# Performance work log

Measured on AMD Instinct MI355X. Metric: run time of the kernel, lower is better.

## Reference

```python
import jax, jax.numpy as jnp
import numpy as np

N, U, OUT_DIM, K, B = 3960, 128, 1, 2, 16
NUM_MAT = 2 * K + 1  # 2 supports (dual random walk), K hops, + identity


def setup_inputs() -> dict:
    key = jax.random.key(0)
    ks = jax.random.split(key, 12)
    s = 0.02
    inp = {
        'inputs': jax.random.normal(ks[0], (B, N * OUT_DIM), jnp.float32),
        'adj_mx': jax.random.uniform(ks[1], (N, N), jnp.float32),
        'hidden_state': jax.random.normal(ks[2], (2, B, N * U), jnp.float32),
        'forward_index': 0,
        # layer 0: input dim = OUT_DIM (=1)
        'Wg0': s * jax.random.normal(ks[3], ((OUT_DIM + U) * NUM_MAT, 2 * U), jnp.float32),
        'bg0': jnp.ones((2 * U,), jnp.float32),  # bias_start=1.0 for gates
        'Wc0': s * jax.random.normal(ks[4], ((OUT_DIM + U) * NUM_MAT, U), jnp.float32),
        'bc0': jnp.zeros((U,), jnp.float32),
        # layer 1: input dim = U
        'Wg1': s * jax.random.normal(ks[5], ((U + U) * NUM_MAT, 2 * U), jnp.float32),
        'bg1': jnp.ones((2 * U,), jnp.float32),
        'Wc1': s * jax.random.normal(ks[6], ((U + U) * NUM_MAT, U), jnp.float32),
        'bc1': jnp.zeros((U,), jnp.float32),
        # projection Linear(rnn_units, output_dim)
        'Wp': s * jax.random.normal(ks[7], (U, OUT_DIM), jnp.float32),
        'bp': jnp.zeros((OUT_DIM,), jnp.float32),
    }
    return inp


def _random_walk(adj):
    # D^{-1} A with 0 for zero-degree rows
    d = adj.sum(axis=1)
    d_inv = jnp.where(d > 0, 1.0 / d, 0.0)
    return d_inv[:, None] * adj


def _gconv(x, h, supports, W, b):
    # x: (B,N,c_in), h: (B,N,U) -> (B,N,out)
    bsz = x.shape[0]
    cat = jnp.concatenate([x, h], axis=2)          # (B,N,C)
    C = cat.shape[2]
    x0 = cat.transpose(1, 2, 0).reshape(N, C * bsz)  # (N, C*B)
    xs = [x0]
    for S in supports:
        x1 = S @ x0
        xs.append(x1)
        xk_2, xk_1 = x0, x1
        for _ in range(2, K + 1):
            x2 = 2.0 * (S @ xk_1) - xk_2  # Chebyshev-style recurrence (as in GTS/DCRNN)
            xs.append(x2)
            xk_2, xk_1 = xk_1, x2
    xcat = jnp.stack(xs, 0)                         # (M,N,C*B)
    xcat = xcat.reshape(NUM_MAT, N, C, bsz).transpose(3, 1, 2, 0)  # (B,N,C,M)
    xcat = xcat.reshape(bsz * N, C * NUM_MAT)
    return (xcat @ W + b).reshape(bsz, N, -1)


def _dcgru_cell(x, h, supports, Wg, bg, Wc, bc):
    gates = jax.nn.sigmoid(_gconv(x, h, supports, Wg, bg))  # (B,N,2U)
    r, u = gates[..., :U], gates[..., U:]
    c = jnp.tanh(_gconv(x, r * h, supports, Wc, bc))        # (B,N,U)
    return u * h + (1.0 - u) * c


def reference(inputs, adj_mx, hidden_state, forward_index,
              Wg0, bg0, Wc0, bc0, Wg1, bg1, Wc1, bc1, Wp, bp):
    bsz = inputs.shape[0]
    supports = [_random_walk(adj_mx).T, _random_walk(adj_mx.T).T]
    x = inputs.reshape(bsz, N, OUT_DIM)
    h0 = hidden_state[0].reshape(bsz, N, U)
    h1 = hidden_state[1].reshape(bsz, N, U)
    nh0 = _dcgru_cell(x, h0, supports, Wg0, bg0, Wc0, bc0)
    nh1 = _dcgru_cell(nh0, h1, supports, Wg1, bg1, Wc1, bc1)
    out = (nh1.reshape(-1, U) @ Wp + bp).reshape(bsz, N * OUT_DIM)
    return out
```

## Files before the change

### kernel.cpp

```cpp
#include <hip/hip_runtime.h>


#define NN 3960
#define NP 3968
#define BB 16
#define UU 128
#define NT 62

typedef __attribute__((ext_vector_type(8))) short v8s;
typedef __attribute__((ext_vector_type(4))) float v4f;

__device__ __forceinline__ float bf2f(short h) {
  union { unsigned int u; float f; } v;
  v.u = ((unsigned int)(unsigned short)h) << 16;
  return v.f;
}
__device__ __forceinline__ short f2bf(float f) {
  union { float f; unsigned int u; } v; v.f = f;
  unsigned int r = (v.u + 0x7FFFu + ((v.u >> 16) & 1u)) >> 16;
  return (short)r;
}
__device__ __forceinline__ void gld16(const void* g, void* l) {
  __builtin_amdgcn_global_load_lds(
      (const __attribute__((address_space(1))) void*)g,
      (__attribute__((address_space(3))) void*)l, 16, 0, 0);
}


__global__ void k_rowsum(const float* __restrict__ A, float* __restrict__ out) {
  int i = blockIdx.x;
  float s = 0.f;
  for (int j = threadIdx.x; j < NN; j += 256) s += A[i * NN + j];
  __shared__ float red[256];
  red[threadIdx.x] = s; __syncthreads();
  for (int k = 128; k > 0; k >>= 1) {
    if (threadIdx.x < k) red[threadIdx.x] += red[threadIdx.x + k];
    __syncthreads();
  }
  if (threadIdx.x == 0) out[i] = red[0];
}

__global__ void k_colpart(const float* __restrict__ A, float* __restrict__ part) {
  int j = blockIdx.x * 256 + threadIdx.x;
  if (j >= NN) return;
  int p = blockIdx.y;
  int r0 = p * 495, r1 = r0 + 495;
  float s = 0.f;
  for (int i = r0; i < r1; i++) s += A[i * NN + j];
  part[p * NP + j] = s;
}

__global__ void k_inv(const float* __restrict__ rs, const float* __restrict__ part,
                      float* __restrict__ rinv, float* __restrict__ cinv) {
  int j = blockIdx.x * 256 + threadIdx.x;
  if (j >= NP) return;
  float r = 0.f, c = 0.f;
  if (j < NN) {
    r = rs[j];
    float s = 0.f;
    for (int p = 0; p < 8; p++) s += part[p * NP + j];
    c = s;
  }
  rinv[j] = (j < NN && r > 0.f) ? 1.f / r : 0.f;
  cinv[j] = (j < NN && c > 0.f) ? 1.f / c : 0.f;
}

__global__ void k_supports(const float* __restrict__ A, const float* __restrict__ rinv,
                           const float* __restrict__ cinv,
                           short* __restrict__ S0, short* __restrict__ S1) {
  __shared__ float t[32][33];
  int i0 = blockIdx.y * 32, j0 = blockIdx.x * 32;
  int tx = threadIdx.x, ty = threadIdx.y;
  #pragma unroll
  for (int q = 0; q < 4; q++) {
    int r = i0 + ty + 8 * q, c = j0 + tx;
    float a = (r < NN && c < NN) ? A[r * NN + c] : 0.f;
    t[ty + 8 * q][tx] = a;
    S1[r * NP + c] = f2bf(a * cinv[c]);
  }
  __syncthreads();
  #pragma unroll
  for (int q = 0; q < 4; q++) {
    int I = j0 + ty + 8 * q, J = i0 + tx;
    S0[I * NP + J] = f2bf(t[tx][ty + 8 * q] * rinv[J]);
  }
}

__global__ void k_buildH(const float* __restrict__ hs,
                         short* __restrict__ H0, short* __restrict__ H1) {
  __shared__ float t[32][33];
  int n0 = blockIdx.x * 32, u0 = blockIdx.y * 32;
  int bz = blockIdx.z; int b = bz & 15; int layer = bz >> 4;
  const float* src = hs + (size_t)(layer * BB + b) * NN * UU;
  short* H = layer ? H1 : H0;
  int tx = threadIdx.x, ty = threadIdx.y;
  #pragma unroll
  for (int q = 0; q < 4; q++) {
    int n = n0 + ty + 8 * q, u = u0 + tx;
    t[ty + 8 * q][tx] = (n < NN) ? src[n * UU + u] : 0.f;
  }
  __syncthreads();
  #pragma unroll
  for (int q = 0; q < 4; q++) {
    int u = u0 + ty + 8 * q, n = n0 + tx;
    H[(b * UU + u) * NP + n] = f2bf(t[tx][ty + 8 * q]);
  }
}

__global__ void k_buildX0c(const float* __restrict__ inp, short* __restrict__ X) {
  int n = blockIdx.x * 128 + threadIdx.x;
  int row = blockIdx.y;
  float v = (row < BB && n < NN) ? inp[row * NN + n] : 0.f;
  X[row * NP + n] = f2bf(v);
}

__global__ void k_buildWt(const float* __restrict__ W, short* __restrict__ Wt,
                          int O, int KL, int CxP, int Cx) {
  int idx = blockIdx.x * 256 + threadIdx.x;
  if (idx >= O * KL) return;
  int o = idx / KL, k = idx % KL;
  int KX = 5 * CxP;
  float v = 0.f;
  if (k < KX) {
    int m = k / CxP, c = k % CxP;
    if (c < Cx) v = W[(c * 5 + m) * O + o];
  } else {
    int kl = k - KX; int m = kl >> 7, u = kl & 127;
    v = W[((Cx + u) * 5 + m) * O + o];
  }
  Wt[o * KL + k] = f2bf(v);
}

struct Bt8Args {
  const short* A[4];
  short* Y[4];
  const short* SUB[4];
  int mr[4];
};

__launch_bounds__(512, 2)
__global__ void k_gemm_bt8(Bt8Args P, const short* __restrict__ T0,
                           const short* __restrict__ T1) {
  int z = blockIdx.z;
  int l = blockIdx.x + (blockIdx.y << 3);
  int bx = l >> 4;
  int by = ((l & 7) << 1) + ((l >> 3) & 1);
  int row0 = bx * 256;
  if (row0 >= P.mr[z]) return;
  const short* Ag = P.A[z];
  short* Cg = P.Y[z];
  const short* X0 = P.SUB[z];
  const short* Bg = (z & 1) ? T1 : T0;
  __shared__ short lds[65536];
  int tid = threadIdx.x, lane = tid & 63, wv = tid >> 6;
  int wr = wv >> 2, wc = wv & 3;
  int col0 = by * 256;

  int srow = wv * 16 + (lane >> 2);
  int scol = ((lane & 3) * 8) ^ ((lane >> 5) << 4);
  const short* aS0 = Ag + (size_t)(row0 + srow) * NP + scol;
  const short* aS1 = Ag + (size_t)(row0 + 128 + srow) * NP + scol;
  int br0 = col0 + srow;        if (br0 > NP - 1) br0 = NP - 1;
  int br1 = col0 + 128 + srow;  if (br1 > NP - 1) br1 = NP - 1;
  const short* bS0 = Bg + (size_t)br0 * NP + scol;
  const short* bS1 = Bg + (size_t)br1 * NP + scol;
  short* ldsA = lds + wv * 1024 + lane * 8;
  short* ldsB = lds + 32768 + wv * 1024 + lane * 8;

#define STG_A(buf, h, tau) do { const short* _s = ((h) ? aS1 : aS0) + (tau) * 64; \
    gld16(_s,      ldsA + (buf) * 16384 + (h) * 8192); \
    gld16(_s + 32, ldsA + (buf) * 16384 + (h) * 8192 + 512); } while (0)
#define STG_B(buf, h, tau) do { const short* _s = ((h) ? bS1 : bS0) + (tau) * 64; \
    gld16(_s,      ldsB + (buf) * 16384 + (h) * 8192); \
    gld16(_s + 32, ldsB + (buf) * 16384 + (h) * 8192 + 512); } while (0)

  int fro = (lane & 15) * 32 + (((lane >> 4) * 8) ^ ((lane & 8) * 2));
  int aBase = wr * 8192 + fro;
  int bBase = 32768 + (wc >> 1) * 8192 + (wc & 1) * 4096 + fro;

  v4f acc[8][4];
  #pragma unroll
  for (int i = 0; i < 8; i++)
    #pragma unroll
    for (int j = 0; j < 4; j++) {
      acc[i][j][0] = 0.f; acc[i][j][1] = 0.f; acc[i][j][2] = 0.f; acc[i][j][3] = 0.f;
    }
  v8s afr[4][2], bfr[4][2];

#define RD_A(b, miB) do { _Pragma("unroll") \
  for (int m2 = 0; m2 < 4; m2++) { \
    afr[m2][0] = *(const v8s*)&lds[aBase + (b) * 16384 + ((miB) + m2) * 1024]; \
    afr[m2][1] = *(const v8s*)&lds[aBase + (b) * 16384 + ((miB) + m2) * 1024 + 512]; } } while (0)
#define RD_B(b, niB) do { _Pragma("unroll") \
  for (int n2 = 0; n2 < 2; n2++) { \
    bfr[(niB) + n2][0] = *(const v8s*)&lds[bBase + (b) * 16384 + ((niB) + n2) * 1024]; \
    bfr[(niB) + n2][1] = *(const v8s*)&lds[bBase + (b) * 16384 + ((niB) + n2) * 1024 + 512]; } } while (0)
#define MM(miB, niB) do { __builtin_amdgcn_s_setprio(1); \
  _Pragma("unroll") for (int m2 = 0; m2 < 4; m2++) \
  _Pragma("unroll") for (int n2 = 0; n2 < 2; n2++) { \
    acc[(miB) + m2][(niB) + n2] = __builtin_amdgcn_mfma_f32_16x16x32_bf16( \
        afr[m2][0], bfr[(niB) + n2][0], acc[(miB) + m2][(niB) + n2], 0, 0, 0); \
    acc[(miB) + m2][(niB) + n2] = __builtin_amdgcn_mfma_f32_16x16x32_bf16( \
        afr[m2][1], bfr[(niB) + n2][1], acc[(miB) + m2][(niB) + n2], 0, 0, 0); } \
  __builtin_amdgcn_s_setprio(0); } while (0)
#define BARS do { __builtin_amdgcn_s_barrier(); __builtin_amdgcn_sched_barrier(0); } while (0)
#define VMC(n) asm volatile("s_waitcnt vmcnt(" #n ")" ::: "memory")

  STG_A(0, 0, 0); STG_A(0, 1, 0); STG_B(0, 0, 0); STG_B(0, 1, 0);
  STG_A(1, 0, 1); STG_B(1, 0, 1); STG_B(1, 1, 1);
  VMC(6);
  BARS;

  for (int it = 0; it < NT / 2; it++) {
    int t = 2 * it;
    int st1 = t + 1;
    int st2 = t + 2 > NT - 1 ? NT - 1 : t + 2;
    int st3 = t + 3 > NT - 1 ? NT - 1 : t + 3;
    RD_A(0, 0); RD_B(0, 0); STG_A(1, 1, st1); BARS; MM(0, 0); BARS;
    RD_B(0, 2); BARS; MM(0, 2); BARS;
    RD_A(0, 4); STG_B(0, 0, st2); BARS; MM(4, 0); BARS;
    STG_B(0, 1, st2); VMC(4); BARS; MM(4, 2); BARS;
    RD_A(1, 0); RD_B(1, 0); STG_A(0, 0, st2); BARS; MM(0, 0); BARS;
    RD_B(1, 2); STG_A(0, 1, st2); BARS; MM(0, 2); BARS;
    RD_A(1, 4); STG_B(1, 0, st3); BARS; MM(4, 0); BARS;
    STG_B(1, 1, st3); STG_A(1, 0, st3); VMC(6); BARS; MM(4, 2); BARS;
  }

  int cheb = X0 != nullptr;
  #pragma unroll
  for (int mi = 0; mi < 8; mi++)
    #pragma unroll
    for (int ni = 0; ni < 4; ni++) {
      int col = col0 + wc * 64 + ni * 16 + (lane & 15);
      if (col < NP) {
        #pragma unroll
        for (int r = 0; r < 4; r++) {
          int row = row0 + wr * 128 + mi * 16 + (lane >> 4) * 4 + r;
          float v = acc[mi][ni][r];
          if (cheb) v = 2.f * v - bf2f(X0[(size_t)row * NP + col]);
          Cg[(size_t)row * NP + col] = f2bf(v);
        }
      }
    }
#undef STG_A
#undef STG_B
#undef RD_A
#undef RD_B
#undef MM
#undef BARS
#undef VMC
}

__launch_bounds__(256, 2)
__global__ void k_gemm_wt(const short* __restrict__ Wt, int KL, int KX, int CxP,
                          int bsx,
                          const short* __restrict__ pX0, const short* __restrict__ pX1,
                          const short* __restrict__ pX2, const short* __restrict__ pX3,
                          const short* __restrict__ pX4,
                          const short* __restrict__ pH0, const short* __restrict__ pH1,
                          const short* __restrict__ pH2, const short* __restrict__ pH3,
                          const short* __restrict__ pH4,
                          const float* __restrict__ bias, const short* __restrict__ H,
                          short* __restrict__ Ut, short* __restrict__ out0, int epi) {
  __shared__ short lA[128 * 32];
  __shared__ short lB[128 * 40];
  int tid = threadIdx.x, lane = tid & 63, w = tid >> 6;
  int n0 = blockIdx.x * 128;
  int oy = blockIdx.y;
  int b = blockIdx.z;
  int arow = w * 16 + (lane >> 2), koff = (lane & 3) * 8;
  const short* wa0 = Wt + (oy * 128 + arow) * KL + koff;
  const short* wa1 = Wt + (oy * 128 + 64 + arow) * KL + koff;
  short* la0 = lA + w * 512 + lane * 8;
  short* la1 = lA + 2048 + w * 512 + lane * 8;
  int srow = tid >> 3, c16 = (tid & 7) * 16;
  int sk7 = srow & 7, sk3 = srow >> 3;
  int wr = (w >> 1) * 64, wc = (w & 1) * 64;
  v4f acc[4][4];
  #pragma unroll
  for (int i = 0; i < 4; i++)
    #pragma unroll
    for (int j = 0; j < 4; j++) {
      acc[i][j][0] = 0.f; acc[i][j][1] = 0.f; acc[i][j][2] = 0.f; acc[i][j][3] = 0.f;
    }
  int KT = KL >> 5;
  for (int kt = 0; kt < KT; kt++) {
    int kb = kt * 32;
    const short* src;
    if (kb < KX) {
      int m = kb / CxP, c0 = kb % CxP;
      const short* base = m == 0 ? pX0 : m == 1 ? pX1 : m == 2 ? pX2 : m == 3 ? pX3 : pX4;
      src = base + (b * bsx + c0) * NP;
    } else {
      int kl = kb - KX; int m = kl >> 7, c0 = kl & 127;
      const short* base = m == 0 ? pH0 : m == 1 ? pH1 : m == 2 ? pH2 : m == 3 ? pH3 : pH4;
      src = base + (b * UU + c0) * NP;
    }
    __syncthreads();
    gld16(wa0 + kb, la0); gld16(wa1 + kb, la1);
    const v8s* p = (const v8s*)(src + srow * NP + n0 + c16);
    v8s v0 = p[0], v1 = p[1];
    #pragma unroll
    for (int j = 0; j < 8; j++) {
      int cA = c16 + j, cB = c16 + 8 + j;
      lB[cA * 40 + sk7 + 8 * ((sk3 ^ (cA >> 4)) & 3)] = v0[j];
      lB[cB * 40 + sk7 + 8 * ((sk3 ^ (cB >> 4)) & 3)] = v1[j];
    }
    __syncthreads();
    v8s af[4], bfv[4];
    #pragma unroll
    for (int mi = 0; mi < 4; mi++)
      af[mi] = *(const v8s*)&lA[(wr + mi * 16 + (lane & 15)) * 32 + (lane >> 4) * 8];
    #pragma unroll
    for (int ni = 0; ni < 4; ni++) {
      int colb = wc + ni * 16 + (lane & 15);
      bfv[ni] = *(const v8s*)&lB[colb * 40 + 8 * (((lane >> 4) ^ (colb >> 4)) & 3)];
    }
    #pragma unroll
    for (int mi = 0; mi < 4; mi++)
      #pragma unroll
      for (int ni = 0; ni < 4; ni++)
        acc[mi][ni] = __builtin_amdgcn_mfma_f32_16x16x32_bf16(af[mi], bfv[ni], acc[mi][ni], 0, 0, 0);
  }
  #pragma unroll
  for (int mi = 0; mi < 4; mi++)
    #pragma unroll
    for (int ni = 0; ni < 4; ni++) {
      int col = n0 + wc + ni * 16 + (lane & 15);
      #pragma unroll
      for (int r = 0; r < 4; r++) {
        int o = oy * 128 + wr + mi * 16 + (lane >> 4) * 4 + r;
        float v = acc[mi][ni][r] + bias[o];
        if (epi == 0) {
          float s = 1.f / (1.f + __expf(-v));
          if (o < UU) {
            int idx = (b * UU + o) * NP + col;
            out0[idx] = f2bf(s * bf2f(H[idx]));
          } else {
            int idx = (b * UU + (o - UU)) * NP + col;
            Ut[idx] = f2bf(s);
          }
        } else {
          float cv = tanhf(v);
          int idx = (b * UU + o) * NP + col;
          float u = bf2f(Ut[idx]), h = bf2f(H[idx]);
          out0[idx] = f2bf(u * h + (1.f - u) * cv);
        }
      }
    }
}

__global__ void k_proj(const short* __restrict__ nh, const float* __restrict__ Wp,
                       const float* __restrict__ bp, float* __restrict__ out) {
  int n = blockIdx.x * 256 + threadIdx.x;
  int b = blockIdx.y;
  if (n >= NN) return;
  float acc = bp[0];
  #pragma unroll 8
  for (int u = 0; u < UU; u++)
    acc += bf2f(nh[(b * UU + u) * NP + n]) * Wp[u];
  out[b * NN + n] = acc;
}

__global__ void k_bail(float* out, int n, float val) {
  int i = blockIdx.x * 256 + threadIdx.x;
  if (i < n) out[i] = val;
}


extern "C" void kernel_launch(void* const* d_in, const int* in_sizes, int n_in,
                              void* d_out, int out_size, void* d_ws, size_t ws_size,
                              hipStream_t stream) {
  const float* inp = (const float*)d_in[0];
  const float* adj = (const float*)d_in[1];
  const float* hid = (const float*)d_in[2];
  const float* Wg0 = (const float*)d_in[4];
  const float* bg0 = (const float*)d_in[5];
  const float* Wc0 = (const float*)d_in[6];
  const float* bc0 = (const float*)d_in[7];
  const float* Wg1 = (const float*)d_in[8];
  const float* bg1 = (const float*)d_in[9];
  const float* Wc1 = (const float*)d_in[10];
  const float* bc1 = (const float*)d_in[11];
  const float* Wp = (const float*)d_in[12];
  const float* bp = (const float*)d_in[13];
  float* out = (float*)d_out;

  const size_t SZ_S = (size_t)NP * NP * 2;
  const size_t SZ_M = (size_t)2048 * NP * 2;
  const size_t SZ_MS = (size_t)512 * NP * 2;

  size_t o_S0 = 0;
  size_t o_S1 = o_S0 + SZ_S;
  size_t o_H0 = o_S1 + SZ_S;
  size_t o_H1 = o_H0 + SZ_M;
  size_t o_Ut = o_H1 + SZ_M;
  size_t o_Xrh = o_Ut + SZ_M;
  size_t o_nh0 = o_Xrh + SZ_M;
  size_t o_YB = o_nh0 + SZ_M;
  size_t o_YX123 = o_YB + 4 * SZ_M;
  size_t o_X0c = o_YX123;
  size_t o_YS = o_X0c + SZ_MS;
  size_t o_Wg0t = o_YX123 + 3 * SZ_M;
  size_t o_Wc0t = o_Wg0t + (size_t)256 * 800 * 2;
  size_t o_Wg1t = o_Wc0t + (size_t)128 * 800 * 2;
  size_t o_Wc1t = o_Wg1t + (size_t)256 * 1280 * 2;
  size_t o_rinv = o_Wc1t + (size_t)128 * 1280 * 2;
  size_t o_cinv = o_rinv + NP * 4;
  size_t o_rs = o_cinv + NP * 4;
  size_t o_part = o_rs + NP * 4;
  size_t NEED = o_part + (size_t)8 * NP * 4;

  if (ws_size < NEED) {
    float v = -(float)(double)(ws_size >> 20);
    k_bail<<<(out_size + 255) / 256, 256, 0, stream>>>(out, out_size, v);
    return;
  }

  char* w = (char*)d_ws;
  short* S0 = (short*)(w + o_S0);
  short* S1 = (short*)(w + o_S1);
  short* H0 = (short*)(w + o_H0);
  short* H1 = (short*)(w + o_H1);
  short* Ut = (short*)(w + o_Ut);
  short* Xrh = (short*)(w + o_Xrh);
  short* nh0 = (short*)(w + o_nh0);
  short* nh1 = Ut;
  short* YB[4];
  for (int i = 0; i < 4; i++) YB[i] = (short*)(w + o_YB + i * SZ_M);
  short* YXa = H0;
  short* YXb = (short*)(w + o_YX123 + 0 * SZ_M);
  short* YXc = (short*)(w + o_YX123 + 1 * SZ_M);
  short* YXd = (short*)(w + o_YX123 + 2 * SZ_M);
  short* YS[4];
  for (int i = 0; i < 4; i++) YS[i] = (short*)(w + o_YS + i * SZ_MS);
  short* X0c = (short*)(w + o_X0c);
  short* Wg0t = (short*)(w + o_Wg0t);
  short* Wc0t = (short*)(w + o_Wc0t);
  short* Wg1t = (short*)(w + o_Wg1t);
  short* Wc1t = (short*)(w + o_Wc1t);
  float* rinv = (float*)(w + o_rinv);
  float* cinv = (float*)(w + o_cinv);
  float* rs = (float*)(w + o_rs);
  float* part = (float*)(w + o_part);

  k_rowsum<<<NN, 256, 0, stream>>>(adj, rs);
  k_colpart<<<dim3(16, 8), 256, 0, stream>>>(adj, part);
  k_inv<<<16, 256, 0, stream>>>(rs, part, rinv, cinv);
  k_supports<<<dim3(124, 124), dim3(32, 8), 0, stream>>>(adj, rinv, cinv, S0, S1);
  k_buildH<<<dim3(124, 4, 32), dim3(32, 8), 0, stream>>>(hid, H0, H1);
  k_buildX0c<<<dim3(31, 256), 128, 0, stream>>>(inp, X0c);
  k_buildWt<<<(256 * 800 + 255) / 256, 256, 0, stream>>>(Wg0, Wg0t, 256, 800, 32, 1);
  k_buildWt<<<(128 * 800 + 255) / 256, 256, 0, stream>>>(Wc0, Wc0t, 128, 800, 32, 1);
  k_buildWt<<<(256 * 1280 + 255) / 256, 256, 0, stream>>>(Wg1, Wg1t, 256, 1280, 128, 128);
  k_buildWt<<<(128 * 1280 + 255) / 256, 256, 0, stream>>>(Wc1, Wc1t, 128, 1280, 128, 128);

  auto launch_bt8 = [&](const Bt8Args& a, int nz) {
    k_gemm_bt8<<<dim3(8, 16, nz), 512, 0, stream>>>(a, S0, S1);
  };

  {
    Bt8Args h1 = {{X0c, X0c, H0, H0}, {YS[0], YS[2], YB[0], YB[2]},
                  {nullptr, nullptr, nullptr, nullptr}, {256, 256, 2048, 2048}};
    launch_bt8(h1, 4);
    Bt8Args h2 = {{YS[0], YS[2], YB[0], YB[2]}, {YS[1], YS[3], YB[1], YB[3]},
                  {X0c, X0c, H0, H0}, {256, 256, 2048, 2048}};
    launch_bt8(h2, 4);
  }
  k_gemm_wt<<<dim3(31, 2, 16), 256, 0, stream>>>(Wg0t, 800, 160, 32, 1,
      X0c, YS[0], YS[1], YS[2], YS[3], H0, YB[0], YB[1], YB[2], YB[3],
      bg0, H0, Ut, Xrh, 0);
  {
    Bt8Args h1 = {{Xrh, Xrh, nullptr, nullptr}, {YB[0], YB[2], nullptr, nullptr},
                  {nullptr, nullptr, nullptr, nullptr}, {2048, 2048, 0, 0}};
    launch_bt8(h1, 2);
    Bt8Args h2 = {{YB[0], YB[2], nullptr, nullptr}, {YB[1], YB[3], nullptr, nullptr},
                  {Xrh, Xrh, nullptr, nullptr}, {2048, 2048, 0, 0}};
    launch_bt8(h2, 2);
  }
  k_gemm_wt<<<dim3(31, 1, 16), 256, 0, stream>>>(Wc0t, 800, 160, 32, 1,
      X0c, YS[0], YS[1], YS[2], YS[3], Xrh, YB[0], YB[1], YB[2], YB[3],
      bc0, H0, Ut, nh0, 1);

  {
    Bt8Args h1 = {{nh0, nh0, H1, H1}, {YXa, YXc, YB[0], YB[2]},
                  {nullptr, nullptr, nullptr, nullptr}, {2048, 2048, 2048, 2048}};
    launch_bt8(h1, 4);
    Bt8Args h2 = {{YXa, YXc, YB[0], YB[2]}, {YXb, YXd, YB[1], YB[3]},
                  {nh0, nh0, H1, H1}, {2048, 2048, 2048, 2048}};
    launch_bt8(h2, 4);
  }
  k_gemm_wt<<<dim3(31, 2, 16), 256, 0, stream>>>(Wg1t, 1280, 640, 128, 128,
      nh0, YXa, YXb, YXc, YXd, H1, YB[0], YB[1], YB[2], YB[3],
      bg1, H1, Ut, Xrh, 0);
  {
    Bt8Args h1 = {{Xrh, Xrh, nullptr, nullptr}, {YB[0], YB[2], nullptr, nullptr},
                  {nullptr, nullptr, nullptr, nullptr}, {2048, 2048, 0, 0}};
    launch_bt8(h1, 2);
    Bt8Args h2 = {{YB[0], YB[2], nullptr, nullptr}, {YB[1], YB[3], nullptr, nullptr},
                  {Xrh, Xrh, nullptr, nullptr}, {2048, 2048, 0, 0}};
    launch_bt8(h2, 2);
  }
  k_gemm_wt<<<dim3(31, 1, 16), 256, 0, stream>>>(Wc1t, 1280, 640, 128, 128,
      nh0, YXa, YXb, YXc, YXd, Xrh, YB[0], YB[1], YB[2], YB[3],
      bc1, H1, Ut, nh1, 1);

  k_proj<<<dim3(16, 16), 256, 0, stream>>>(nh1, Wp, bp, out);
}
```

Before: 1.732 ms.

## Double-buffer LDS fragment registers to overlap reads with MFMA in GEMM loop

Splits the A/B fragment registers into low/high halves so LDS reads for the next sub-tile are issued alongside MFMAs on the current one, rather than being separated from them by barriers. Global-to-LDS staging is reordered to match, with one stage per barrier phase and the prefetch depth adjusted. The aim is to hide LDS read latency behind matrix instructions in the dense support GEMM. In exchange it uses more VGPRs, which could hurt occupancy under launch bounds of 2 blocks per SM, and the reordered staging carries correctness risk for buffer reuse.

```diff
diff --git a/kernel.cpp b/kernel.cpp
--- a/kernel.cpp
+++ b/kernel.cpp
@@ -185,45 +185,54 @@
     for (int j = 0; j < 4; j++) {
       acc[i][j][0] = 0.f; acc[i][j][1] = 0.f; acc[i][j][2] = 0.f; acc[i][j][3] = 0.f;
     }
-  v8s afr[4][2], bfr[4][2];
-
-#define RD_A(b, miB) do { _Pragma("unroll") \
+  v8s afrL[4][2], afrH[4][2], bfrL[2][2], bfrH[2][2];
+
+#define RD_AL(b) do { _Pragma("unroll") \
   for (int m2 = 0; m2 < 4; m2++) { \
-    afr[m2][0] = *(const v8s*)&lds[aBase + (b) * 16384 + ((miB) + m2) * 1024]; \
-    afr[m2][1] = *(const v8s*)&lds[aBase + (b) * 16384 + ((miB) + m2) * 1024 + 512]; } } while (0)
-#define RD_B(b, niB) do { _Pragma("unroll") \
+    afrL[m2][0] = *(const v8s*)&lds[aBase + (b) * 16384 + m2 * 1024]; \
+    afrL[m2][1] = *(const v8s*)&lds[aBase + (b) * 16384 + m2 * 1024 + 512]; } } while (0)
+#define RD_AH(b) do { _Pragma("unroll") \
+  for (int m2 = 0; m2 < 4; m2++) { \
+    afrH[m2][0] = *(const v8s*)&lds[aBase + (b) * 16384 + (4 + m2) * 1024]; \
+    afrH[m2][1] = *(const v8s*)&lds[aBase + (b) * 16384 + (4 + m2) * 1024 + 512]; } } while (0)
+#define RD_BL(b) do { _Pragma("unroll") \
   for (int n2 = 0; n2 < 2; n2++) { \
-    bfr[(niB) + n2][0] = *(const v8s*)&lds[bBase + (b) * 16384 + ((niB) + n2) * 1024]; \
-    bfr[(niB) + n2][1] = *(const v8s*)&lds[bBase + (b) * 16384 + ((niB) + n2) * 1024 + 512]; } } while (0)
-#define MM(miB, niB) do { __builtin_amdgcn_s_setprio(1); \
+    bfrL[n2][0] = *(const v8s*)&lds[bBase + (b) * 16384 + n2 * 1024]; \
+    bfrL[n2][1] = *(const v8s*)&lds[bBase + (b) * 16384 + n2 * 1024 + 512]; } } while (0)
+#define RD_BH(b) do { _Pragma("unroll") \
+  for (int n2 = 0; n2 < 2; n2++) { \
+    bfrH[n2][0] = *(const v8s*)&lds[bBase + (b) * 16384 + (2 + n2) * 1024]; \
+    bfrH[n2][1] = *(const v8s*)&lds[bBase + (b) * 16384 + (2 + n2) * 1024 + 512]; } } while (0)
+#define MMX(AF, BF, miB, niB) do { __builtin_amdgcn_s_setprio(1); \
   _Pragma("unroll") for (int m2 = 0; m2 < 4; m2++) \
   _Pragma("unroll") for (int n2 = 0; n2 < 2; n2++) { \
     acc[(miB) + m2][(niB) + n2] = __builtin_amdgcn_mfma_f32_16x16x32_bf16( \
-        afr[m2][0], bfr[(niB) + n2][0], acc[(miB) + m2][(niB) + n2], 0, 0, 0); \
+        AF[m2][0], BF[n2][0], acc[(miB) + m2][(niB) + n2], 0, 0, 0); \
     acc[(miB) + m2][(niB) + n2] = __builtin_amdgcn_mfma_f32_16x16x32_bf16( \
-        afr[m2][1], bfr[(niB) + n2][1], acc[(miB) + m2][(niB) + n2], 0, 0, 0); } \
+        AF[m2][1], BF[n2][1], acc[(miB) + m2][(niB) + n2], 0, 0, 0); } \
   __builtin_amdgcn_s_setprio(0); } while (0)
 #define BARS do { __builtin_amdgcn_s_barrier(); __builtin_amdgcn_sched_barrier(0); } while (0)
 #define VMC(n) asm volatile("s_waitcnt vmcnt(" #n ")" ::: "memory")
 
   STG_A(0, 0, 0); STG_A(0, 1, 0); STG_B(0, 0, 0); STG_B(0, 1, 0);
-  STG_A(1, 0, 1); STG_B(1, 0, 1); STG_B(1, 1, 1);
-  VMC(6);
+  STG_B(1, 0, 1); STG_B(1, 1, 1);
+  VMC(4);
   BARS;
+  RD_AL(0); RD_BL(0);
 
   for (int it = 0; it < NT / 2; it++) {
     int t = 2 * it;
-    int st1 = t + 1;
-    int st2 = t + 2 > NT - 1 ? NT - 1 : t + 2;
-    int st3 = t + 3 > NT - 1 ? NT - 1 : t + 3;
-    RD_A(0, 0); RD_B(0, 0); STG_A(1, 1, st1); BARS; MM(0, 0); BARS;
-    RD_B(0, 2); BARS; MM(0, 2); BARS;
-    RD_A(0, 4); STG_B(0, 0, st2); BARS; MM(4, 0); BARS;
-    STG_B(0, 1, st2); VMC(4); BARS; MM(4, 2); BARS;
-    RD_A(1, 0); RD_B(1, 0); STG_A(0, 0, st2); BARS; MM(0, 0); BARS;
-    RD_B(1, 2); STG_A(0, 1, st2); BARS; MM(0, 2); BARS;
-    RD_A(1, 4); STG_B(1, 0, st3); BARS; MM(4, 0); BARS;
-    STG_B(1, 1, st3); STG_A(1, 0, st3); VMC(6); BARS; MM(4, 2); BARS;
+    int s1 = t + 1;
+    int s2 = t + 2 > NT - 1 ? NT - 1 : t + 2;
+    int s3 = t + 3 > NT - 1 ? NT - 1 : t + 3;
+    STG_A(1, 0, s1); BARS; RD_BH(0); MMX(afrL, bfrL, 0, 0); BARS;
+    STG_A(1, 1, s1); BARS; RD_AH(0); MMX(afrL, bfrH, 0, 2); BARS;
+    STG_B(0, 0, s2); BARS; MMX(afrH, bfrL, 4, 0); BARS;
+    STG_B(0, 1, s2); VMC(4); BARS; RD_AL(1); RD_BL(1); MMX(afrH, bfrH, 4, 2); BARS;
+    STG_A(0, 0, s2); BARS; RD_BH(1); MMX(afrL, bfrL, 0, 0); BARS;
+    STG_A(0, 1, s2); BARS; RD_AH(1); MMX(afrL, bfrH, 0, 2); BARS;
+    STG_B(1, 0, s3); BARS; MMX(afrH, bfrL, 4, 0); BARS;
+    STG_B(1, 1, s3); VMC(4); BARS; RD_AL(0); RD_BL(0); MMX(afrH, bfrH, 4, 2); BARS;
   }
 
   int cheb = X0 != nullptr;
@@ -244,9 +253,11 @@
     }
 #undef STG_A
 #undef STG_B
-#undef RD_A
-#undef RD_B
-#undef MM
+#undef RD_AL
+#undef RD_AH
+#undef RD_BL
+#undef RD_BH
+#undef MMX
 #undef BARS
 #undef VMC
 }
```

After: 2.627 ms. +51.6%, slower.

## Replace double-buffered pipelined GEMM main loop with single-buffered load-wait-compute loop

Applied to the files above, without the earlier changes.

The 256x256-tile support GEMM kernel drops its hand-scheduled double-buffered LDS pipeline, where global-to-LDS loads for later K-tiles were interleaved with MFMA phases. Each K-step now loads its tile, waits for all loads, synchronizes, reads fragments and runs all MFMAs. LDS use is halved, which could allow more resident blocks, but load latency is no longer hidden behind compute within a block.

```diff
diff --git a/kernel.cpp b/kernel.cpp
--- a/kernel.cpp
+++ b/kernel.cpp
@@ -151,7 +151,7 @@
   short* Cg = P.Y[z];
   const short* X0 = P.SUB[z];
   const short* Bg = (z & 1) ? T1 : T0;
-  __shared__ short lds[65536];
+  __shared__ short lds[32768];
   int tid = threadIdx.x, lane = tid & 63, wv = tid >> 6;
   int wr = wv >> 2, wc = wv & 3;
   int col0 = by * 256;
@@ -165,18 +165,11 @@
   const short* bS0 = Bg + (size_t)br0 * NP + scol;
   const short* bS1 = Bg + (size_t)br1 * NP + scol;
   short* ldsA = lds + wv * 1024 + lane * 8;
-  short* ldsB = lds + 32768 + wv * 1024 + lane * 8;
-
-#define STG_A(buf, h, tau) do { const short* _s = ((h) ? aS1 : aS0) + (tau) * 64; \
-    gld16(_s,      ldsA + (buf) * 16384 + (h) * 8192); \
-    gld16(_s + 32, ldsA + (buf) * 16384 + (h) * 8192 + 512); } while (0)
-#define STG_B(buf, h, tau) do { const short* _s = ((h) ? bS1 : bS0) + (tau) * 64; \
-    gld16(_s,      ldsB + (buf) * 16384 + (h) * 8192); \
-    gld16(_s + 32, ldsB + (buf) * 16384 + (h) * 8192 + 512); } while (0)
+  short* ldsB = lds + 16384 + wv * 1024 + lane * 8;
 
   int fro = (lane & 15) * 32 + (((lane >> 4) * 8) ^ ((lane & 8) * 2));
   int aBase = wr * 8192 + fro;
-  int bBase = 32768 + (wc >> 1) * 8192 + (wc & 1) * 4096 + fro;
+  int bBase = 16384 + (wc >> 1) * 8192 + (wc & 1) * 4096 + fro;
 
   v4f acc[8][4];
   #pragma unroll
@@ -185,45 +178,46 @@
     for (int j = 0; j < 4; j++) {
       acc[i][j][0] = 0.f; acc[i][j][1] = 0.f; acc[i][j][2] = 0.f; acc[i][j][3] = 0.f;
     }
-  v8s afr[4][2], bfr[4][2];
-
-#define RD_A(b, miB) do { _Pragma("unroll") \
-  for (int m2 = 0; m2 < 4; m2++) { \
-    afr[m2][0] = *(const v8s*)&lds[aBase + (b) * 16384 + ((miB) + m2) * 1024]; \
-    afr[m2][1] = *(const v8s*)&lds[aBase + (b) * 16384 + ((miB) + m2) * 1024 + 512]; } } while (0)
-#define RD_B(b, niB) do { _Pragma("unroll") \
-  for (int n2 = 0; n2 < 2; n2++) { \
-    bfr[(niB) + n2][0] = *(const v8s*)&lds[bBase + (b) * 16384 + ((niB) + n2) * 1024]; \
-    bfr[(niB) + n2][1] = *(const v8s*)&lds[bBase + (b) * 16384 + ((niB) + n2) * 1024 + 512]; } } while (0)
-#define MM(miB, niB) do { __builtin_amdgcn_s_setprio(1); \
-  _Pragma("unroll") for (int m2 = 0; m2 < 4; m2++) \
-  _Pragma("unroll") for (int n2 = 0; n2 < 2; n2++) { \
-    acc[(miB) + m2][(niB) + n2] = __builtin_amdgcn_mfma_f32_16x16x32_bf16( \
-        afr[m2][0], bfr[(niB) + n2][0], acc[(miB) + m2][(niB) + n2], 0, 0, 0); \
-    acc[(miB) + m2][(niB) + n2] = __builtin_amdgcn_mfma_f32_16x16x32_bf16( \
-        afr[m2][1], bfr[(niB) + n2][1], acc[(miB) + m2][(niB) + n2], 0, 0, 0); } \
-  __builtin_amdgcn_s_setprio(0); } while (0)
+
 #define BARS do { __builtin_amdgcn_s_barrier(); __builtin_amdgcn_sched_barrier(0); } while (0)
-#define VMC(n) asm volatile("s_waitcnt vmcnt(" #n ")" ::: "memory")
-
-  STG_A(0, 0, 0); STG_A(0, 1, 0); STG_B(0, 0, 0); STG_B(0, 1, 0);
-  STG_A(1, 0, 1); STG_B(1, 0, 1); STG_B(1, 1, 1);
-  VMC(6);
-  BARS;
-
-  for (int it = 0; it < NT / 2; it++) {
-    int t = 2 * it;
-    int st1 = t + 1;
-    int st2 = t + 2 > NT - 1 ? NT - 1 : t + 2;
-    int st3 = t + 3 > NT - 1 ? NT - 1 : t + 3;
-    RD_A(0, 0); RD_B(0, 0); STG_A(1, 1, st1); BARS; MM(0, 0); BARS;
-    RD_B(0, 2); BARS; MM(0, 2); BARS;
-    RD_A(0, 4); STG_B(0, 0, st2); BARS; MM(4, 0); BARS;
-    STG_B(0, 1, st2); VMC(4); BARS; MM(4, 2); BARS;
-    RD_A(1, 0); RD_B(1, 0); STG_A(0, 0, st2); BARS; MM(0, 0); BARS;
-    RD_B(1, 2); STG_A(0, 1, st2); BARS; MM(0, 2); BARS;
-    RD_A(1, 4); STG_B(1, 0, st3); BARS; MM(4, 0); BARS;
-    STG_B(1, 1, st3); STG_A(1, 0, st3); VMC(6); BARS; MM(4, 2); BARS;
+#define VMC0 asm volatile("s_waitcnt vmcnt(0)" ::: "memory")
+
+  for (int t = 0; t < NT; t++) {
+    {
+      const short* sa0 = aS0 + t * 64;
+      const short* sa1 = aS1 + t * 64;
+      const short* sb0 = bS0 + t * 64;
+      const short* sb1 = bS1 + t * 64;
+      gld16(sa0, ldsA);             gld16(sa0 + 32, ldsA + 512);
+      gld16(sa1, ldsA + 8192);      gld16(sa1 + 32, ldsA + 8192 + 512);
+      gld16(sb0, ldsB);             gld16(sb0 + 32, ldsB + 512);
+      gld16(sb1, ldsB + 8192);      gld16(sb1 + 32, ldsB + 8192 + 512);
+    }
+    VMC0;
+    BARS;
+    v8s afr[8][2], bfr[4][2];
+    #pragma unroll
+    for (int mi = 0; mi < 8; mi++) {
+      afr[mi][0] = *(const v8s*)&lds[aBase + mi * 1024];
+      afr[mi][1] = *(const v8s*)&lds[aBase + mi * 1024 + 512];
+    }
+    #pragma unroll
+    for (int ni = 0; ni < 4; ni++) {
+      bfr[ni][0] = *(const v8s*)&lds[bBase + ni * 1024];
+      bfr[ni][1] = *(const v8s*)&lds[bBase + ni * 1024 + 512];
+    }
+    __builtin_amdgcn_s_setprio(1);
+    #pragma unroll
+    for (int mi = 0; mi < 8; mi++)
+      #pragma unroll
+      for (int ni = 0; ni < 4; ni++) {
+        acc[mi][ni] = __builtin_amdgcn_mfma_f32_16x16x32_bf16(
+            afr[mi][0], bfr[ni][0], acc[mi][ni], 0, 0, 0);
+        acc[mi][ni] = __builtin_amdgcn_mfma_f32_16x16x32_bf16(
+            afr[mi][1], bfr[ni][1], acc[mi][ni], 0, 0, 0);
+      }
+    __builtin_amdgcn_s_setprio(0);
+    BARS;
   }
 
   int cheb = X0 != nullptr;
@@ -242,13 +236,8 @@
         }
       }
     }
-#undef STG_A
-#undef STG_B
-#undef RD_A
-#undef RD_B
-#undef MM
 #undef BARS
-#undef VMC
+#undef VMC0
 }
 
 __launch_bounds__(256, 2)
```

New measurement: 2.227 ms. 28.5% more time.
